# Kernel tuning notes

Measured on AMD Instinct MI355X. Metric: run time of the kernel, lower is better.

## Reference

```python
import jax, jax.numpy as jnp
import numpy as np

LAMBDA_COORD = 5.0
LAMBDA_NOOBJ = 0.5
EPS = 1e-16


def setup_inputs() -> dict:
    key = jax.random.key(0)
    k1, k2, k3 = jax.random.split(key, 3)
    B, H, W, C, T = 64, 80, 80, 80, 50
    predictions = jax.random.normal(k1, (B, H * W, 5 + C), dtype=jnp.float32)
    cls_id = jax.random.randint(k2, (B, T), 0, C).astype(jnp.float32)
    # cx, cy, w, h normalized to (0,1); margin keeps every target in-grid
    boxes = jax.random.uniform(k3, (B, T, 4), minval=0.05, maxval=0.95, dtype=jnp.float32)
    targets = jnp.concatenate([cls_id[..., None], boxes], axis=-1)  # [B, T, 5]
    return {"predictions": predictions, "targets": targets, "H": H, "W": W}


def reference(predictions, targets, H, W):
    B, HW, D = predictions.shape
    T = targets.shape[1]
    num_classes = D - 5

    cls_id = targets[..., 0].astype(jnp.int32)           # [B, T]
    cx, cy = targets[..., 1], targets[..., 2]
    w, h = targets[..., 3], targets[..., 4]

    # grid assignment (all targets in-bounds by construction)
    gx = jnp.floor(cx * W).astype(jnp.int32)
    gy = jnp.floor(cy * H).astype(jnp.int32)
    gi = gy * W + gx                                     # [B, T] flat cell index

    tx = cx * W - gx
    ty = cy * H - gy
    tw = jnp.log(w * W + EPS)
    th = jnp.log(h * H + EPS)

    # gather predictions at assigned cells -> [B, T, D]
    g = jnp.take_along_axis(predictions, gi[:, :, None], axis=1)
    pred_xy = jax.nn.sigmoid(g[..., :2])
    pred_wh = g[..., 2:4]
    pred_cls = g[..., 5:]

    # per-target MSE (mean over the 2 coords, as F.mse_loss), summed over targets
    xy_loss = jnp.sum(jnp.mean((pred_xy - jnp.stack([tx, ty], axis=-1)) ** 2, axis=-1))
    wh_loss = jnp.sum(jnp.mean((pred_wh - jnp.stack([tw, th], axis=-1)) ** 2, axis=-1))

    # per-target cross entropy, summed
    logp = jax.nn.log_softmax(pred_cls, axis=-1)
    cls_loss = -jnp.sum(jnp.take_along_axis(logp, cls_id[..., None], axis=-1))

    # objectness masks via scatter
    obj_mask = jnp.zeros((B, HW), dtype=bool).at[jnp.arange(B)[:, None], gi].set(True)
    noobj_mask = ~obj_mask

    conf_logit = predictions[..., 4]                     # [B, HW]
    # BCE(sigmoid(x), 1) = softplus(-x); BCE(sigmoid(x), 0) = softplus(x)
    n_obj_cells = jnp.sum(obj_mask)
    n_noobj = jnp.sum(noobj_mask)
    conf_obj = jnp.sum(jax.nn.softplus(-conf_logit) * obj_mask) / jnp.maximum(n_obj_cells, 1)
    conf_noobj = jnp.sum(jax.nn.softplus(conf_logit) * noobj_mask) / jnp.maximum(n_noobj, 1)

    num_obj = max(B * T, 1)  # all targets valid
    total = (LAMBDA_COORD * (xy_loss + wh_loss) / num_obj
             + conf_obj / num_obj
             + LAMBDA_NOOBJ * conf_noobj / jnp.maximum(n_noobj, 1)
             + cls_loss / num_obj)
    return total
```

## Files before the change

### kernel.cpp

```cpp
#include <hip/hip_runtime.h>
#include <math.h>

#define NB    64
#define NH    80
#define NW    80
#define NHW   6400
#define NT    50
#define ND    85
#define NCELL (NB * NHW)
#define NTGT  (NB * NT)
#define GRID2 1600

__device__ __forceinline__ float softplus_f(float x) {
    return fmaxf(x, 0.0f) + log1pf(expf(-fabsf(x)));
}

__global__ __launch_bounds__(256)
void main_kernel(const float* __restrict__ pred,
                 const float* __restrict__ tgt,
                 float* __restrict__ partials) {
    const int bid  = blockIdx.x;
    const int tid  = threadIdx.x;
    const int lane = tid & 63;
    const int wib  = tid >> 6;

    __shared__ float s_red[6];
    if (tid < 6) s_red[tid] = 0.0f;

    const int c = bid * 256 + tid;
    const float conf_v = pred[(size_t)c * ND + 4];

    __syncthreads();

    if (bid < 800) {
        const int i = bid * 4 + wib;
        const int b = i / NT;
        const int t = i - b * NT;

        const float* tp = tgt + (size_t)i * 5;
        float cx = tp[1];
        float cy = tp[2];
        int gx = (int)floorf(cx * (float)NW);
        int gy = (int)floorf(cy * (float)NH);
        int gi = gy * NW + gx;

        bool match = false;
        if (lane < t) {
            const float* tj = tgt + ((size_t)b * NT + lane) * 5;
            int gxj = (int)floorf(tj[1] * (float)NW);
            int gyj = (int)floorf(tj[2] * (float)NH);
            match = (gyj * NW + gxj) == gi;
        }
        unsigned long long mb = __ballot(match);

        const float* g = pred + ((size_t)b * NHW + gi) * ND;
        float e0 = g[lane];
        float e1 = (lane < ND - 64) ? g[64 + lane] : 0.0f;

        float s = ((lane >= 5)      ? expf(e0) : 0.0f)
                + ((lane < ND - 64) ? expf(e1) : 0.0f);
        #pragma unroll
        for (int off = 32; off; off >>= 1) s += __shfl_xor(s, off, 64);

        if (lane == 0) {
            int   cid  = (int)tp[0];
            float w    = tp[3];
            float h    = tp[4];
            float gsel = g[5 + cid];
            float g0 = g[0], g1 = g[1], g2 = g[2], g3 = g[3], confp = g[4];

            float cls_v = -(gsel - logf(s));

            float px = 1.0f / (1.0f + expf(-g0));
            float py = 1.0f / (1.0f + expf(-g1));
            float tx = cx * (float)NW - (float)gx;
            float ty = cy * (float)NH - (float)gy;
            float tw = logf(w * (float)NW + 1e-16f);
            float th = logf(h * (float)NH + 1e-16f);
            float xy = 0.5f * ((px - tx) * (px - tx) + (py - ty) * (py - ty));
            float wh = 0.5f * ((g2 - tw) * (g2 - tw) + (g3 - th) * (g3 - th));

            atomicAdd(&s_red[0], xy + wh);
            atomicAdd(&s_red[1], cls_v);
            if (mb == 0ull) {
                atomicAdd(&s_red[2], softplus_f(-confp));
                atomicAdd(&s_red[3], 1.0f);
                atomicAdd(&s_red[4], softplus_f(confp));
            }
        }
    }

    {
        float sp = softplus_f(conf_v);
        #pragma unroll
        for (int off = 32; off; off >>= 1) sp += __shfl_xor(sp, off, 64);
        if (lane == 0) atomicAdd(&s_red[5], sp);
    }

    __syncthreads();
    if (tid < 6) partials[(size_t)bid * 6 + tid] = s_red[tid];
}

__global__ __launch_bounds__(1024)
void final_kernel(const float* __restrict__ partials,
                  float* __restrict__ out) {
    const int tid  = threadIdx.x;
    const int lane = tid & 63;
    const int wib  = tid >> 6;

    float a[6] = {0, 0, 0, 0, 0, 0};
    for (int r = tid; r < GRID2; r += 1024) {
        #pragma unroll
        for (int k = 0; k < 6; ++k) a[k] += partials[(size_t)r * 6 + k];
    }
    #pragma unroll
    for (int k = 0; k < 6; ++k) {
        #pragma unroll
        for (int off = 32; off; off >>= 1) a[k] += __shfl_xor(a[k], off, 64);
    }

    __shared__ float sh[16][6];
    if (lane == 0) {
        #pragma unroll
        for (int k = 0; k < 6; ++k) sh[wib][k] = a[k];
    }
    __syncthreads();

    if (tid == 0) {
        float t0 = 0, t1 = 0, t2 = 0, t3 = 0, t4 = 0, t5 = 0;
        #pragma unroll
        for (int wv = 0; wv < 16; ++wv) {
            t0 += sh[wv][0]; t1 += sh[wv][1]; t2 += sh[wv][2];
            t3 += sh[wv][3]; t4 += sh[wv][4]; t5 += sh[wv][5];
        }
        float coord = t0, cls = t1, objs = t2, nobj = t3, corr = t4, allsp = t5;

        float noobj = allsp - corr;
        float nno   = (float)NCELL - nobj;

        float conf_obj   = objs  / fmaxf(nobj, 1.0f);
        float conf_noobj = noobj / fmaxf(nno,  1.0f);
        const float num_obj = (float)(NB * NT);

        out[0] = 5.0f * coord / num_obj
               + conf_obj / num_obj
               + 0.5f * conf_noobj / fmaxf(nno, 1.0f)
               + cls / num_obj;
    }
}

extern "C" void kernel_launch(void* const* d_in, const int* in_sizes, int n_in,
                              void* d_out, int out_size, void* d_ws, size_t ws_size,
                              hipStream_t stream) {
    const float* pred = (const float*)d_in[0];
    const float* tgt  = (const float*)d_in[1];
    float* partials   = (float*)d_ws;

    main_kernel <<<GRID2, 256, 0, stream>>>(pred, tgt, partials);
    final_kernel<<<1,    1024, 0, stream>>>(partials, (float*)d_out);
}
```

Before: 20.67 us.

## Fuse final reduction into main kernel via last-block atomic counter

After: 37.06 us. 79.3% more time.

```diff
diff --git a/kernel.cpp b/kernel.cpp
--- a/kernel.cpp
+++ b/kernel.cpp
@@ -9,30 +9,34 @@
 #define ND    85
 #define NCELL (NB * NHW)
 #define NTGT  (NB * NT)
-#define GRID2 1600
+#define GRID  800
+
+__device__ float g_acc[6] = {0.f, 0.f, 0.f, 0.f, 0.f, 0.f};
+__device__ int   g_cnt = 0;
 
 __device__ __forceinline__ float softplus_f(float x) {
     return fmaxf(x, 0.0f) + log1pf(expf(-fabsf(x)));
 }
 
 __global__ __launch_bounds__(256)
-void main_kernel(const float* __restrict__ pred,
-                 const float* __restrict__ tgt,
-                 float* __restrict__ partials) {
+void fused_kernel(const float* __restrict__ pred,
+                  const float* __restrict__ tgt,
+                  float* __restrict__ out) {
     const int bid  = blockIdx.x;
     const int tid  = threadIdx.x;
     const int lane = tid & 63;
     const int wib  = tid >> 6;
 
     __shared__ float s_red[6];
+
+    const int c0 = bid * 512 + tid;
+    const float cva = pred[(size_t)c0 * ND + 4];
+    const float cvb = pred[((size_t)c0 + 256) * ND + 4];
+
     if (tid < 6) s_red[tid] = 0.0f;
-
-    const int c = bid * 256 + tid;
-    const float conf_v = pred[(size_t)c * ND + 4];
-
     __syncthreads();
 
-    if (bid < 800) {
+    {
         const int i = bid * 4 + wib;
         const int b = i / NT;
         const int t = i - b * NT;
@@ -91,61 +95,48 @@
     }
 
     {
-        float sp = softplus_f(conf_v);
+        float sp = softplus_f(cva) + softplus_f(cvb);
         #pragma unroll
         for (int off = 32; off; off >>= 1) sp += __shfl_xor(sp, off, 64);
         if (lane == 0) atomicAdd(&s_red[5], sp);
     }
 
     __syncthreads();
-    if (tid < 6) partials[(size_t)bid * 6 + tid] = s_red[tid];
-}
 
-__global__ __launch_bounds__(1024)
-void final_kernel(const float* __restrict__ partials,
-                  float* __restrict__ out) {
-    const int tid  = threadIdx.x;
-    const int lane = tid & 63;
-    const int wib  = tid >> 6;
-
-    float a[6] = {0, 0, 0, 0, 0, 0};
-    for (int r = tid; r < GRID2; r += 1024) {
-        #pragma unroll
-        for (int k = 0; k < 6; ++k) a[k] += partials[(size_t)r * 6 + k];
-    }
-    #pragma unroll
-    for (int k = 0; k < 6; ++k) {
-        #pragma unroll
-        for (int off = 32; off; off >>= 1) a[k] += __shfl_xor(a[k], off, 64);
-    }
-
-    __shared__ float sh[16][6];
-    if (lane == 0) {
-        #pragma unroll
-        for (int k = 0; k < 6; ++k) sh[wib][k] = a[k];
-    }
+    if (tid < 6) atomicAdd(&g_acc[tid], s_red[tid]);
     __syncthreads();
 
     if (tid == 0) {
-        float t0 = 0, t1 = 0, t2 = 0, t3 = 0, t4 = 0, t5 = 0;
-        #pragma unroll
-        for (int wv = 0; wv < 16; ++wv) {
-            t0 += sh[wv][0]; t1 += sh[wv][1]; t2 += sh[wv][2];
-            t3 += sh[wv][3]; t4 += sh[wv][4]; t5 += sh[wv][5];
+        __threadfence();
+        int old = atomicAdd(&g_cnt, 1);
+        if (old == GRID - 1) {
+            float coord = atomicAdd(&g_acc[0], 0.0f);
+            float cls   = atomicAdd(&g_acc[1], 0.0f);
+            float objs  = atomicAdd(&g_acc[2], 0.0f);
+            float nobj  = atomicAdd(&g_acc[3], 0.0f);
+            float corr  = atomicAdd(&g_acc[4], 0.0f);
+            float allsp = atomicAdd(&g_acc[5], 0.0f);
+
+            float noobj = allsp - corr;
+            float nno   = (float)NCELL - nobj;
+
+            float conf_obj   = objs  / fmaxf(nobj, 1.0f);
+            float conf_noobj = noobj / fmaxf(nno,  1.0f);
+            const float num_obj = (float)(NB * NT);
+
+            out[0] = 5.0f * coord / num_obj
+                   + conf_obj / num_obj
+                   + 0.5f * conf_noobj / fmaxf(nno, 1.0f)
+                   + cls / num_obj;
+
+            atomicExch(&g_acc[0], 0.0f);
+            atomicExch(&g_acc[1], 0.0f);
+            atomicExch(&g_acc[2], 0.0f);
+            atomicExch(&g_acc[3], 0.0f);
+            atomicExch(&g_acc[4], 0.0f);
+            atomicExch(&g_acc[5], 0.0f);
+            atomicExch(&g_cnt, 0);
         }
-        float coord = t0, cls = t1, objs = t2, nobj = t3, corr = t4, allsp = t5;
-
-        float noobj = allsp - corr;
-        float nno   = (float)NCELL - nobj;
-
-        float conf_obj   = objs  / fmaxf(nobj, 1.0f);
-        float conf_noobj = noobj / fmaxf(nno,  1.0f);
-        const float num_obj = (float)(NB * NT);
-
-        out[0] = 5.0f * coord / num_obj
-               + conf_obj / num_obj
-               + 0.5f * conf_noobj / fmaxf(nno, 1.0f)
-               + cls / num_obj;
     }
 }
 
@@ -154,8 +145,5 @@
                               hipStream_t stream) {
     const float* pred = (const float*)d_in[0];
     const float* tgt  = (const float*)d_in[1];
-    float* partials   = (float*)d_ws;
-
-    main_kernel <<<GRID2, 256, 0, stream>>>(pred, tgt, partials);
-    final_kernel<<<1,    1024, 0, stream>>>(partials, (float*)d_out);
+    fused_kernel<<<GRID, 256, 0, stream>>>(pred, tgt, (float*)d_out);
 }
```

## Remap work to 512 blocks of 1024 threads and transpose partials layout

Applied to the files above, without the earlier changes.

New measurement: 18.44 us. -10.8%, faster.

```diff
diff --git a/kernel.cpp b/kernel.cpp
--- a/kernel.cpp
+++ b/kernel.cpp
@@ -9,13 +9,14 @@
 #define ND    85
 #define NCELL (NB * NHW)
 #define NTGT  (NB * NT)
-#define GRID2 1600
+#define GRID  512
+#define CPB   800
 
 __device__ __forceinline__ float softplus_f(float x) {
     return fmaxf(x, 0.0f) + log1pf(expf(-fabsf(x)));
 }
 
-__global__ __launch_bounds__(256)
+__global__ __launch_bounds__(1024)
 void main_kernel(const float* __restrict__ pred,
                  const float* __restrict__ tgt,
                  float* __restrict__ partials) {
@@ -26,14 +27,10 @@
 
     __shared__ float s_red[6];
     if (tid < 6) s_red[tid] = 0.0f;
-
-    const int c = bid * 256 + tid;
-    const float conf_v = pred[(size_t)c * ND + 4];
-
     __syncthreads();
 
-    if (bid < 800) {
-        const int i = bid * 4 + wib;
+    if (wib < 6 || (wib == 6 && bid < 128)) {
+        const int i = (wib < 6) ? (bid * 6 + wib) : (3072 + bid);
         const int b = i / NT;
         const int t = i - b * NT;
 
@@ -59,67 +56,68 @@
 
         float s = ((lane >= 5)      ? expf(e0) : 0.0f)
                 + ((lane < ND - 64) ? expf(e1) : 0.0f);
+
+        int   cid  = (int)tp[0];
+        float w    = tp[3];
+        float h    = tp[4];
+        float gsel = g[5 + cid];
+        float g0 = g[0], g1 = g[1], g2 = g[2], g3 = g[3], confp = g[4];
+
+        float px = 1.0f / (1.0f + expf(-g0));
+        float py = 1.0f / (1.0f + expf(-g1));
+        float tx = cx * (float)NW - (float)gx;
+        float ty = cy * (float)NH - (float)gy;
+        float tw = logf(w * (float)NW + 1e-16f);
+        float th = logf(h * (float)NH + 1e-16f);
+        float xy = 0.5f * ((px - tx) * (px - tx) + (py - ty) * (py - ty));
+        float wh = 0.5f * ((g2 - tw) * (g2 - tw) + (g3 - th) * (g3 - th));
+        float sp_n = softplus_f(-confp);
+        float sp_p = softplus_f(confp);
+
         #pragma unroll
         for (int off = 32; off; off >>= 1) s += __shfl_xor(s, off, 64);
 
         if (lane == 0) {
-            int   cid  = (int)tp[0];
-            float w    = tp[3];
-            float h    = tp[4];
-            float gsel = g[5 + cid];
-            float g0 = g[0], g1 = g[1], g2 = g[2], g3 = g[3], confp = g[4];
-
             float cls_v = -(gsel - logf(s));
-
-            float px = 1.0f / (1.0f + expf(-g0));
-            float py = 1.0f / (1.0f + expf(-g1));
-            float tx = cx * (float)NW - (float)gx;
-            float ty = cy * (float)NH - (float)gy;
-            float tw = logf(w * (float)NW + 1e-16f);
-            float th = logf(h * (float)NH + 1e-16f);
-            float xy = 0.5f * ((px - tx) * (px - tx) + (py - ty) * (py - ty));
-            float wh = 0.5f * ((g2 - tw) * (g2 - tw) + (g3 - th) * (g3 - th));
-
             atomicAdd(&s_red[0], xy + wh);
             atomicAdd(&s_red[1], cls_v);
             if (mb == 0ull) {
-                atomicAdd(&s_red[2], softplus_f(-confp));
+                atomicAdd(&s_red[2], sp_n);
                 atomicAdd(&s_red[3], 1.0f);
-                atomicAdd(&s_red[4], softplus_f(confp));
+                atomicAdd(&s_red[4], sp_p);
             }
         }
     }
 
-    {
-        float sp = softplus_f(conf_v);
+    if (wib < 13) {
+        const int c = bid * CPB + tid;
+        float sp = (tid < CPB) ? softplus_f(pred[(size_t)c * ND + 4]) : 0.0f;
         #pragma unroll
         for (int off = 32; off; off >>= 1) sp += __shfl_xor(sp, off, 64);
         if (lane == 0) atomicAdd(&s_red[5], sp);
     }
 
     __syncthreads();
-    if (tid < 6) partials[(size_t)bid * 6 + tid] = s_red[tid];
+    if (tid < 6) partials[(size_t)tid * GRID + bid] = s_red[tid];
 }
 
-__global__ __launch_bounds__(1024)
+__global__ __launch_bounds__(512)
 void final_kernel(const float* __restrict__ partials,
                   float* __restrict__ out) {
     const int tid  = threadIdx.x;
     const int lane = tid & 63;
     const int wib  = tid >> 6;
 
-    float a[6] = {0, 0, 0, 0, 0, 0};
-    for (int r = tid; r < GRID2; r += 1024) {
-        #pragma unroll
-        for (int k = 0; k < 6; ++k) a[k] += partials[(size_t)r * 6 + k];
-    }
+    float a[6];
+    #pragma unroll
+    for (int k = 0; k < 6; ++k) a[k] = partials[(size_t)k * GRID + tid];
     #pragma unroll
     for (int k = 0; k < 6; ++k) {
         #pragma unroll
         for (int off = 32; off; off >>= 1) a[k] += __shfl_xor(a[k], off, 64);
     }
 
-    __shared__ float sh[16][6];
+    __shared__ float sh[8][6];
     if (lane == 0) {
         #pragma unroll
         for (int k = 0; k < 6; ++k) sh[wib][k] = a[k];
@@ -129,7 +127,7 @@
     if (tid == 0) {
         float t0 = 0, t1 = 0, t2 = 0, t3 = 0, t4 = 0, t5 = 0;
         #pragma unroll
-        for (int wv = 0; wv < 16; ++wv) {
+        for (int wv = 0; wv < 8; ++wv) {
             t0 += sh[wv][0]; t1 += sh[wv][1]; t2 += sh[wv][2];
             t3 += sh[wv][3]; t4 += sh[wv][4]; t5 += sh[wv][5];
         }
@@ -156,6 +154,6 @@
     const float* tgt  = (const float*)d_in[1];
     float* partials   = (float*)d_ws;
 
-    main_kernel <<<GRID2, 256, 0, stream>>>(pred, tgt, partials);
-    final_kernel<<<1,    1024, 0, stream>>>(partials, (float*)d_out);
+    main_kernel <<<GRID, 1024, 0, stream>>>(pred, tgt, partials);
+    final_kernel<<<1,     512, 0, stream>>>(partials, (float*)d_out);
 }
```
